# Optimization experiments

Hardware: AMD Instinct MI355X
Metric: run time of the kernel (lower is better)

## Reference

```python
import jax, jax.numpy as jnp
import numpy as np

EMBED = 1024
HEADS = 16
HEAD_DIM = 64
FF = 4096
EPS = 1e-5


def _layernorm(x, g, b):
    mu = jnp.mean(x, axis=-1, keepdims=True)
    var = jnp.mean(jnp.square(x - mu), axis=-1, keepdims=True)
    return (x - mu) * jax.lax.rsqrt(var + EPS) * g + b


def setup_inputs() -> dict:
    key = jax.random.key(0)
    ks = jax.random.split(key, 12)
    s_in = 1.0 / np.sqrt(EMBED)
    s_hd = 1.0 / np.sqrt(HEADS * HEAD_DIM)
    s_ff = 1.0 / np.sqrt(FF)
    return {
        "x": jax.random.normal(ks[0], (4, 2048, EMBED), dtype=jnp.float32),
        "Wq": jax.random.uniform(ks[1], (HEADS, EMBED, HEAD_DIM), jnp.float32, -s_in, s_in),
        "Wk": jax.random.uniform(ks[2], (HEADS, EMBED, HEAD_DIM), jnp.float32, -s_in, s_in),
        "Wv": jax.random.uniform(ks[3], (HEADS, EMBED, HEAD_DIM), jnp.float32, -s_in, s_in),
        "Wo": jax.random.uniform(ks[4], (HEADS * HEAD_DIM, EMBED), jnp.float32, -s_hd, s_hd),
        "bo": jax.random.uniform(ks[5], (EMBED,), jnp.float32, -s_hd, s_hd),
        "W1": jax.random.uniform(ks[6], (EMBED, FF), jnp.float32, -s_in, s_in),
        "b1": jax.random.uniform(ks[7], (FF,), jnp.float32, -s_in, s_in),
        "W2": jax.random.uniform(ks[8], (FF, EMBED), jnp.float32, -s_ff, s_ff),
        "b2": jax.random.uniform(ks[9], (EMBED,), jnp.float32, -s_ff, s_ff),
        "ln1_g": jnp.ones((EMBED,), jnp.float32),
        "ln1_b": jnp.zeros((EMBED,), jnp.float32),
        "ln2_g": jnp.ones((EMBED,), jnp.float32),
        "ln2_b": jnp.zeros((EMBED,), jnp.float32),
    }


def reference(x, Wq, Wk, Wv, Wo, bo, W1, b1, W2, b2, ln1_g, ln1_b, ln2_g, ln2_b):
    B, T, C = x.shape
    h = _layernorm(x, ln1_g, ln1_b)
    # per-head projections, batched over heads: [B,H,T,Dh]
    q = jnp.einsum("btc,hcd->bhtd", h, Wq)
    k = jnp.einsum("btc,hcd->bhtd", h, Wk)
    v = jnp.einsum("btc,hcd->bhtd", h, Wv)
    scale = HEAD_DIM ** -0.5
    att = jnp.einsum("bhtd,bhsd->bhts", q, k) * scale  # [B,H,T,T]
    causal = jnp.tril(jnp.ones((T, T), dtype=bool))
    att = jnp.where(causal, att, -jnp.inf)
    att = jax.nn.softmax(att, axis=-1)
    out = jnp.einsum("bhts,bhsd->bhtd", att, v)  # [B,H,T,Dh]
    # concat heads (matches torch.cat over head outputs) -> [B,T,H*Dh]
    out = out.transpose(0, 2, 1, 3).reshape(B, T, HEADS * HEAD_DIM)
    x = x + out @ Wo + bo
    h2 = _layernorm(x, ln2_g, ln2_b)
    ff = jax.nn.relu(h2 @ W1 + b1) @ W2 + b2
    return x + ff
```

## Files before the change

kernel.cpp:

```cpp
#include <hip/hip_runtime.h>
#include <hip/hip_bf16.h>

#define EMBED 1024
#define HEADS 16
#define HEAD_DIM 64
#define FFDIM 4096
#define TSEQ 2048
#define BATCH 4
#define ROWS (BATCH * TSEQ)

typedef __bf16 bf16;
typedef __attribute__((ext_vector_type(8))) __bf16 bf16x8;
typedef __attribute__((ext_vector_type(4))) __bf16 bf16x4;
typedef __attribute__((ext_vector_type(4))) float f32x4;

typedef const __attribute__((address_space(1))) void* gvp;
typedef __attribute__((address_space(3))) void* svp;

__global__ __launch_bounds__(256) void conv_wqkv_t(
    const float* __restrict__ Wq, const float* __restrict__ Wk,
    const float* __restrict__ Wv, bf16* __restrict__ WqkvT) {
  __shared__ bf16 t[64][72];
  int tid = threadIdx.x;
  int k0 = blockIdx.x * 64;
  int head = blockIdx.y;
  int which = blockIdx.z;
  const float* src = which == 0 ? Wq : which == 1 ? Wk : Wv;
  float scale = which == 0 ? 0.125f * 1.44269504088896f : 1.0f;
  src += (size_t)head * 65536;
  bf16* dst = WqkvT + ((size_t)which * 1024 + head * 64) * 1024;
#pragma unroll
  for (int i = 0; i < 4; ++i) {
    int r = i * 16 + (tid >> 4);
    int c = (tid & 15) * 4;
    float4 v = *(const float4*)&src[(size_t)(k0 + r) * 64 + c];
    t[c + 0][r] = (bf16)(v.x * scale);
    t[c + 1][r] = (bf16)(v.y * scale);
    t[c + 2][r] = (bf16)(v.z * scale);
    t[c + 3][r] = (bf16)(v.w * scale);
  }
  __syncthreads();
#pragma unroll
  for (int i = 0; i < 2; ++i) {
    int r = i * 32 + (tid >> 3);
    int c = (tid & 7) * 8;
    bf16x8 o;
#pragma unroll
    for (int j = 0; j < 8; ++j) o[j] = t[r][c + j];
    *(bf16x8*)&dst[(size_t)r * 1024 + k0 + c] = o;
  }
}

__global__ __launch_bounds__(256) void transpose_conv(
    const float* __restrict__ W, bf16* __restrict__ WT, int K, int N) {
  __shared__ bf16 t[64][72];
  int tid = threadIdx.x;
  int n0 = blockIdx.x * 64, k0 = blockIdx.y * 64;
#pragma unroll
  for (int i = 0; i < 4; ++i) {
    int r = i * 16 + (tid >> 4);
    int c = (tid & 15) * 4;
    float4 v = *(const float4*)&W[(size_t)(k0 + r) * N + n0 + c];
    t[c + 0][r] = (bf16)v.x;
    t[c + 1][r] = (bf16)v.y;
    t[c + 2][r] = (bf16)v.z;
    t[c + 3][r] = (bf16)v.w;
  }
  __syncthreads();
#pragma unroll
  for (int i = 0; i < 2; ++i) {
    int r = i * 32 + (tid >> 3);
    int c = (tid & 7) * 8;
    bf16x8 o;
#pragma unroll
    for (int j = 0; j < 8; ++j) o[j] = t[r][c + j];
    *(bf16x8*)&WT[(size_t)(n0 + r) * K + k0 + c] = o;
  }
}

__global__ __launch_bounds__(256) void transpose_v(const bf16* __restrict__ v,
                                                   bf16* __restrict__ vt) {
  __shared__ bf16 t[64][72];
  int bh = blockIdx.y;
  int t0 = blockIdx.x * 64;
  const bf16* src = v + (size_t)bh * 131072;
  bf16* dst = vt + (size_t)bh * 131072;
  int tid = threadIdx.x;
#pragma unroll
  for (int i = 0; i < 2; ++i) {
    int c = tid + i * 256;
    int r = c >> 3, d0 = (c & 7) * 8;
    bf16x8 vv = *(const bf16x8*)&src[(size_t)(t0 + r) * 64 + d0];
#pragma unroll
    for (int j = 0; j < 8; ++j) t[d0 + j][r] = vv[j];
  }
  __syncthreads();
#pragma unroll
  for (int i = 0; i < 2; ++i) {
    int c = tid + i * 256;
    int r = c >> 3, s0 = (c & 7) * 8;
    bf16x8 o;
#pragma unroll
    for (int j = 0; j < 8; ++j) o[j] = t[r][s0 + j];
    *(bf16x8*)&dst[(size_t)r * 2048 + t0 + s0] = o;
  }
}

__global__ __launch_bounds__(256) void ln_kernel(
    const float* __restrict__ x, const float* __restrict__ g,
    const float* __restrict__ bta, bf16* __restrict__ out) {
  int row = blockIdx.x;
  const float* xr = x + (size_t)row * EMBED;
  float4 v = ((const float4*)xr)[threadIdx.x];
  float s1 = v.x + v.y + v.z + v.w;
  float s2 = v.x * v.x + v.y * v.y + v.z * v.z + v.w * v.w;
#pragma unroll
  for (int off = 1; off < 64; off <<= 1) {
    s1 += __shfl_xor(s1, off);
    s2 += __shfl_xor(s2, off);
  }
  __shared__ float red[8];
  int wid = threadIdx.x >> 6;
  int lane = threadIdx.x & 63;
  if (lane == 0) {
    red[wid * 2] = s1;
    red[wid * 2 + 1] = s2;
  }
  __syncthreads();
  s1 = red[0] + red[2] + red[4] + red[6];
  s2 = red[1] + red[3] + red[5] + red[7];
  float mu = s1 * (1.0f / EMBED);
  float var = s2 * (1.0f / EMBED) - mu * mu;
  float rs = rsqrtf(var + 1e-5f);
  float4 gv = ((const float4*)g)[threadIdx.x];
  float4 bv = ((const float4*)bta)[threadIdx.x];
  bf16x4 o;
  o[0] = (bf16)((v.x - mu) * rs * gv.x + bv.x);
  o[1] = (bf16)((v.y - mu) * rs * gv.y + bv.y);
  o[2] = (bf16)((v.z - mu) * rs * gv.z + bv.z);
  o[3] = (bf16)((v.w - mu) * rs * gv.w + bv.w);
  *(bf16x4*)(out + (size_t)row * EMBED + threadIdx.x * 4) = o;
}

template <int EPI>
__global__ __launch_bounds__(256) void gemm_bf16(
    const bf16* __restrict__ A, const bf16* __restrict__ BT,
    float* __restrict__ Cf, bf16* __restrict__ Cb,
    const float* __restrict__ bias, const float* __restrict__ resid,
    int M, int N, int K) {
  __shared__ __attribute__((aligned(16))) bf16 As[128 * 32];
  __shared__ __attribute__((aligned(16))) bf16 Bs[128 * 32];
  int gx = gridDim.x;
  int nwg = gx * gridDim.y;
  int wgid = blockIdx.y * gx + blockIdx.x;
  int cpx = nwg >> 3;
  int swz = (wgid & 7) * cpx + (wgid >> 3);
  int m0 = (swz / gx) * 128, n0 = (swz % gx) * 128;
  int tid = threadIdx.x;
  int lane = tid & 63, wid = tid >> 6;
  int lr = lane & 15, lg = lane >> 4;
  int wr = (wid >> 1) * 64, wc = (wid & 1) * 64;
  int srow = lane >> 2;
  int sk = (lane & 3) * 8;
  f32x4 acc[4][4] = {};
  for (int kt = 0; kt < K; kt += 32) {
#pragma unroll
    for (int i = 0; i < 2; ++i) {
      int c = wid * 2 + i;
      int row = c * 16 + srow;
      const bf16* ga = &A[(size_t)(m0 + row) * K + kt + sk];
      const bf16* gb = &BT[(size_t)(n0 + row) * K + kt + sk];
      __builtin_amdgcn_global_load_lds((gvp)(const void*)ga,
                                       (svp)(void*)&As[c * 512], 16, 0, 0);
      __builtin_amdgcn_global_load_lds((gvp)(const void*)gb,
                                       (svp)(void*)&Bs[c * 512], 16, 0, 0);
    }
    __syncthreads();
    bf16x8 af[4], bfr[4];
#pragma unroll
    for (int i = 0; i < 4; ++i) {
      af[i] = *(const bf16x8*)&As[(wr + i * 16 + lr) * 32 + lg * 8];
      bfr[i] = *(const bf16x8*)&Bs[(wc + i * 16 + lr) * 32 + lg * 8];
    }
#pragma unroll
    for (int ar = 0; ar < 4; ++ar)
#pragma unroll
      for (int br = 0; br < 4; ++br)
        acc[ar][br] = __builtin_amdgcn_mfma_f32_16x16x32_bf16(
            af[ar], bfr[br], acc[ar][br], 0, 0, 0);
    __syncthreads();
  }
#pragma unroll
  for (int ar = 0; ar < 4; ++ar) {
#pragma unroll
    for (int br = 0; br < 4; ++br) {
#pragma unroll
      for (int r = 0; r < 4; ++r) {
        int row = m0 + wr + ar * 16 + lg * 4 + r;
        int col = n0 + wc + br * 16 + lr;
        float v = acc[ar][br][r];
        if (EPI == 0) {
          int which = col >> 10, cc = col & 1023;
          int b = row >> 11, t = row & 2047, h = cc >> 6, d = cc & 63;
          bf16* dst = Cb + (size_t)which * 8388608;
          dst[((size_t)((b << 4) + h) * TSEQ + t) * HEAD_DIM + d] = (bf16)v;
        } else if (EPI == 2) {
          size_t o = (size_t)row * N + col;
          Cf[o] = resid[o] + bias[col] + v;
        } else {
          size_t o = (size_t)row * N + col;
          float u = v + bias[col];
          Cb[o] = (bf16)(u > 0.f ? u : 0.f);
        }
      }
    }
  }
}

__global__ __launch_bounds__(256) void attn_kernel(
    const bf16* __restrict__ q, const bf16* __restrict__ k,
    const bf16* __restrict__ vt, bf16* __restrict__ out) {
  __shared__ __attribute__((aligned(16))) bf16 Ks[64][68];
  __shared__ __attribute__((aligned(16))) bf16 Vs[64][68];
  __shared__ __attribute__((aligned(16))) bf16 Ps[4][32][68];
  int bh = blockIdx.x;
  int b = bh >> 4, h = bh & 15;
  const bf16* qb = q + (size_t)bh * TSEQ * HEAD_DIM;
  const bf16* kb = k + (size_t)bh * TSEQ * HEAD_DIM;
  const bf16* vb = vt + (size_t)bh * HEAD_DIM * TSEQ;
  int tid = threadIdx.x, lane = tid & 63, w = tid >> 6;
  int lr = lane & 15, lg = lane >> 4;
  int Q = 15 - blockIdx.y;
  int tw = Q * 128 + w * 32;
  bf16x8 aq[2][2];
#pragma unroll
  for (int rg = 0; rg < 2; ++rg)
#pragma unroll
    for (int kc = 0; kc < 2; ++kc)
      aq[rg][kc] = *(const bf16x8*)&qb[(size_t)(tw + rg * 16 + lr) * HEAD_DIM +
                                       kc * 32 + lg * 8];
  f32x4 o[2][4] = {};
  float lrow[2][4] = {};
  int nj = 2 * Q + 2;
  for (int j = 0; j < nj; ++j) {
#pragma unroll
    for (int i = 0; i < 2; ++i) {
      int c = tid + i * 256;
      int rr = c >> 3, ko = (c & 7) * 8;
      *(bf16x8*)&Ks[rr][ko] =
          *(const bf16x8*)&kb[(size_t)(j * 64 + rr) * HEAD_DIM + ko];
      *(bf16x8*)&Vs[rr][ko] =
          *(const bf16x8*)&vb[(size_t)rr * TSEQ + j * 64 + ko];
    }
    __syncthreads();
    f32x4 s[2][4] = {};
#pragma unroll
    for (int nb = 0; nb < 4; ++nb) {
#pragma unroll
      for (int kc = 0; kc < 2; ++kc) {
        bf16x8 bk = *(const bf16x8*)&Ks[nb * 16 + lr][kc * 32 + lg * 8];
        s[0][nb] = __builtin_amdgcn_mfma_f32_16x16x32_bf16(aq[0][kc], bk,
                                                           s[0][nb], 0, 0, 0);
        s[1][nb] = __builtin_amdgcn_mfma_f32_16x16x32_bf16(aq[1][kc], bk,
                                                           s[1][nb], 0, 0, 0);
      }
    }
    if (j >= 2 * Q) {
#pragma unroll
      for (int rg = 0; rg < 2; ++rg)
#pragma unroll
        for (int nb = 0; nb < 4; ++nb)
#pragma unroll
          for (int r = 0; r < 4; ++r) {
            int sg = j * 64 + nb * 16 + lr;
            int tg = tw + rg * 16 + lg * 4 + r;
            if (sg > tg) s[rg][nb][r] = -1e30f;
          }
    }
#pragma unroll
    for (int rg = 0; rg < 2; ++rg) {
      float p[4][4];
#pragma unroll
      for (int r = 0; r < 4; ++r) {
        float su = 0.f;
#pragma unroll
        for (int nb = 0; nb < 4; ++nb) {
          p[nb][r] = exp2f(s[rg][nb][r] - 8.0f);
          su += p[nb][r];
        }
#pragma unroll
        for (int off = 1; off < 16; off <<= 1) su += __shfl_xor(su, off);
        lrow[rg][r] += su;
      }
#pragma unroll
      for (int nb = 0; nb < 4; ++nb)
#pragma unroll
        for (int r = 0; r < 4; ++r)
          Ps[w][rg * 16 + lg * 4 + r][nb * 16 + lr] = (bf16)p[nb][r];
    }
#pragma unroll
    for (int kc = 0; kc < 2; ++kc) {
      bf16x8 pa0 = *(const bf16x8*)&Ps[w][lr][kc * 32 + lg * 8];
      bf16x8 pa1 = *(const bf16x8*)&Ps[w][16 + lr][kc * 32 + lg * 8];
#pragma unroll
      for (int br = 0; br < 4; ++br) {
        bf16x8 bv = *(const bf16x8*)&Vs[br * 16 + lr][kc * 32 + lg * 8];
        o[0][br] =
            __builtin_amdgcn_mfma_f32_16x16x32_bf16(pa0, bv, o[0][br], 0, 0, 0);
        o[1][br] =
            __builtin_amdgcn_mfma_f32_16x16x32_bf16(pa1, bv, o[1][br], 0, 0, 0);
      }
    }
    __syncthreads();
  }
#pragma unroll
  for (int rg = 0; rg < 2; ++rg)
#pragma unroll
    for (int br = 0; br < 4; ++br)
#pragma unroll
      for (int r = 0; r < 4; ++r) {
        int t = tw + rg * 16 + lg * 4 + r;
        int d = br * 16 + lr;
        float val = o[rg][br][r] / lrow[rg][r];
        out[((size_t)(b * TSEQ) + t) * EMBED + h * HEAD_DIM + d] = (bf16)val;
      }
}

extern "C" void kernel_launch(void* const* d_in, const int* in_sizes, int n_in,
                              void* d_out, int out_size, void* d_ws,
                              size_t ws_size, hipStream_t stream) {
  const float* x = (const float*)d_in[0];
  const float* Wq = (const float*)d_in[1];
  const float* Wk = (const float*)d_in[2];
  const float* Wv = (const float*)d_in[3];
  const float* Wo = (const float*)d_in[4];
  const float* bo = (const float*)d_in[5];
  const float* W1 = (const float*)d_in[6];
  const float* b1 = (const float*)d_in[7];
  const float* W2 = (const float*)d_in[8];
  const float* b2 = (const float*)d_in[9];
  const float* g1 = (const float*)d_in[10];
  const float* be1 = (const float*)d_in[11];
  const float* g2 = (const float*)d_in[12];
  const float* be2 = (const float*)d_in[13];
  float* out = (float*)d_out;
  char* ws = (char*)d_ws;

  const size_t U = 16777216;
  bf16* h = (bf16*)(ws + 0 * U);
  bf16* qb = (bf16*)(ws + 1 * U);
  bf16* vtb = (bf16*)(ws + 0 * U);
  bf16* vnb = (bf16*)(ws + 3 * U);
  bf16* ao = (bf16*)(ws + 3 * U);
  float* x1 = (float*)(ws + 4 * U);
  bf16* h2 = (bf16*)(ws + 6 * U);
  bf16* ff1 = (bf16*)(ws + 0 * U);
  char* wbase = ws + 7 * U;
  bf16* WqkvT = (bf16*)(wbase);
  bf16* WoT = (bf16*)(wbase + 6291456);
  bf16* W1T = (bf16*)(wbase + 8388608);
  bf16* W2T = (bf16*)(wbase + 16777216);

  hipLaunchKernelGGL(conv_wqkv_t, dim3(16, 16, 3), dim3(256), 0, stream, Wq,
                     Wk, Wv, WqkvT);
  hipLaunchKernelGGL(transpose_conv, dim3(16, 16), dim3(256), 0, stream, Wo,
                     WoT, 1024, 1024);
  hipLaunchKernelGGL(transpose_conv, dim3(64, 16), dim3(256), 0, stream, W1,
                     W1T, 1024, 4096);
  hipLaunchKernelGGL(transpose_conv, dim3(16, 64), dim3(256), 0, stream, W2,
                     W2T, 4096, 1024);
  hipLaunchKernelGGL(ln_kernel, dim3(8192), dim3(256), 0, stream, x, g1, be1,
                     h);
  hipLaunchKernelGGL((gemm_bf16<0>), dim3(24, 64), dim3(256), 0, stream, h,
                     WqkvT, (float*)nullptr, qb, (const float*)nullptr,
                     (const float*)nullptr, ROWS, 3072, 1024);
  hipLaunchKernelGGL(transpose_v, dim3(32, 64), dim3(256), 0, stream, vnb,
                     vtb);
  hipLaunchKernelGGL(attn_kernel, dim3(64, 16), dim3(256), 0, stream, qb,
                     qb + 8388608, vtb, ao);
  hipLaunchKernelGGL((gemm_bf16<2>), dim3(8, 64), dim3(256), 0, stream, ao,
                     WoT, x1, (bf16*)nullptr, bo, x, ROWS, 1024, 1024);
  hipLaunchKernelGGL(ln_kernel, dim3(8192), dim3(256), 0, stream, x1, g2, be2,
                     h2);
  hipLaunchKernelGGL((gemm_bf16<3>), dim3(32, 64), dim3(256), 0, stream, h2,
                     W1T, (float*)nullptr, ff1, b1, (const float*)nullptr,
                     ROWS, 4096, 1024);
  hipLaunchKernelGGL((gemm_bf16<2>), dim3(8, 64), dim3(256), 0, stream, ff1,
                     W2T, out, (bf16*)nullptr, b2, x1, ROWS, 1024, 4096);
}
```

Baseline: 465.6 us.

## Add 256x256-tile triple-buffered GEMM with direct-to-LDS loads for QKV and FF1

Adds a new 512-thread GEMM kernel with 256x256 output tiles and a three-stage LDS ring filled by global_load_lds, using an XOR-swizzled layout and raised wave priority around the MFMA block. The QKV projection and the first FFN GEMM now use it, while the older 128x128 kernel is kept only for the residual-add epilogue. The larger tiles raise arithmetic intensity and the deeper pipeline overlaps loads with compute. In exchange the kernel uses 96KB of LDS and many accumulator registers, which limits occupancy. Grids are also small (384 and 512 blocks), so wave quantization across CUs is a risk.

```diff
diff --git a/kernel.cpp b/kernel.cpp
--- a/kernel.cpp
+++ b/kernel.cpp
@@ -143,11 +143,101 @@
 }
 
 template <int EPI>
+__global__ __launch_bounds__(512, 2) void gemm256(
+    const bf16* __restrict__ A, const bf16* __restrict__ BT,
+    bf16* __restrict__ Cb, const float* __restrict__ bias, int M, int N,
+    int K) {
+  __shared__ __attribute__((aligned(16))) char lds[98304];
+  int gx = gridDim.x;
+  int nwg = gx * gridDim.y;
+  int wgid = blockIdx.y * gx + blockIdx.x;
+  int cpx = nwg >> 3;
+  int swz = (wgid & 7) * cpx + (wgid >> 3);
+  int m0 = (swz / gx) * 256, n0 = (swz % gx) * 256;
+  int tid = threadIdx.x;
+  int lane = tid & 63, wid = tid >> 6;
+  int lr = lane & 15, lg = lane >> 4;
+  int wrM = (wid >> 2) * 128;
+  int wcN = (wid & 3) * 64;
+  int crow = lane >> 2;
+  int slotg = (lane & 3) ^ (crow & 3);
+  int NT = K >> 5;
+  size_t rb = (size_t)K * 2;
+
+  auto stageT = [&](int t) {
+    char* dst = lds + ((unsigned)t % 3u) * 32768u;
+#pragma unroll
+    for (int q = 0; q < 2; ++q) {
+      int c = wid * 2 + q;
+      const char* srcA = (const char*)A + (size_t)(m0 + c * 16 + crow) * rb +
+                         (size_t)t * 64 + slotg * 16;
+      __builtin_amdgcn_global_load_lds((gvp)srcA, (svp)(dst + c * 1024), 16, 0,
+                                       0);
+      const char* srcB = (const char*)BT + (size_t)(n0 + c * 16 + crow) * rb +
+                         (size_t)t * 64 + slotg * 16;
+      __builtin_amdgcn_global_load_lds((gvp)srcB, (svp)(dst + 16384 + c * 1024),
+                                       16, 0, 0);
+    }
+  };
+
+  stageT(0);
+  stageT(1);
+  f32x4 acc[8][4] = {};
+  int swcol = ((lg ^ (lr & 3)) * 16);
+  for (int t = 0; t < NT; ++t) {
+    asm volatile("s_waitcnt vmcnt(4)" ::: "memory");
+    __builtin_amdgcn_s_barrier();
+    const char* Ab = lds + ((unsigned)t % 3u) * 32768u;
+    const char* Bb = Ab + 16384;
+    bf16x8 af[8], bfr[4];
+#pragma unroll
+    for (int j = 0; j < 4; ++j)
+      bfr[j] = *(const bf16x8*)(Bb + (wcN + j * 16 + lr) * 64 + swcol);
+#pragma unroll
+    for (int i = 0; i < 8; ++i)
+      af[i] = *(const bf16x8*)(Ab + (wrM + i * 16 + lr) * 64 + swcol);
+    int tn = t + 2;
+    stageT(tn < NT ? tn : tn - NT);
+    __builtin_amdgcn_s_setprio(1);
+#pragma unroll
+    for (int i = 0; i < 8; ++i)
+#pragma unroll
+      for (int j = 0; j < 4; ++j)
+        acc[i][j] = __builtin_amdgcn_mfma_f32_16x16x32_bf16(af[i], bfr[j],
+                                                            acc[i][j], 0, 0, 0);
+    __builtin_amdgcn_s_setprio(0);
+  }
+  asm volatile("s_waitcnt vmcnt(0)" ::: "memory");
+#pragma unroll
+  for (int i = 0; i < 8; ++i) {
+#pragma unroll
+    for (int j = 0; j < 4; ++j) {
+#pragma unroll
+      for (int r = 0; r < 4; ++r) {
+        int row = m0 + wrM + i * 16 + lg * 4 + r;
+        int col = n0 + wcN + j * 16 + lr;
+        float v = acc[i][j][r];
+        if (EPI == 0) {
+          int which = col >> 10, cc = col & 1023;
+          int b = row >> 11, tt = row & 2047, h = cc >> 6, d = cc & 63;
+          bf16* dst = Cb + (size_t)which * 8388608;
+          dst[((size_t)((b << 4) + h) * TSEQ + tt) * HEAD_DIM + d] = (bf16)v;
+        } else {
+          size_t o = (size_t)row * N + col;
+          float u = v + bias[col];
+          Cb[o] = (bf16)(u > 0.f ? u : 0.f);
+        }
+      }
+    }
+  }
+}
+
+template <int EPI>
 __global__ __launch_bounds__(256) void gemm_bf16(
     const bf16* __restrict__ A, const bf16* __restrict__ BT,
     float* __restrict__ Cf, bf16* __restrict__ Cb,
-    const float* __restrict__ bias, const float* __restrict__ resid,
-    int M, int N, int K) {
+    const float* __restrict__ bias, const float* __restrict__ resid, int M,
+    int N, int K) {
   __shared__ __attribute__((aligned(16))) bf16 As[128 * 32];
   __shared__ __attribute__((aligned(16))) bf16 Bs[128 * 32];
   int gx = gridDim.x;
@@ -199,19 +289,8 @@
         int row = m0 + wr + ar * 16 + lg * 4 + r;
         int col = n0 + wc + br * 16 + lr;
         float v = acc[ar][br][r];
-        if (EPI == 0) {
-          int which = col >> 10, cc = col & 1023;
-          int b = row >> 11, t = row & 2047, h = cc >> 6, d = cc & 63;
-          bf16* dst = Cb + (size_t)which * 8388608;
-          dst[((size_t)((b << 4) + h) * TSEQ + t) * HEAD_DIM + d] = (bf16)v;
-        } else if (EPI == 2) {
-          size_t o = (size_t)row * N + col;
-          Cf[o] = resid[o] + bias[col] + v;
-        } else {
-          size_t o = (size_t)row * N + col;
-          float u = v + bias[col];
-          Cb[o] = (bf16)(u > 0.f ? u : 0.f);
-        }
+        size_t o = (size_t)row * N + col;
+        Cf[o] = resid[o] + bias[col] + v;
       }
     }
   }
@@ -371,9 +450,8 @@
                      W2T, 4096, 1024);
   hipLaunchKernelGGL(ln_kernel, dim3(8192), dim3(256), 0, stream, x, g1, be1,
                      h);
-  hipLaunchKernelGGL((gemm_bf16<0>), dim3(24, 64), dim3(256), 0, stream, h,
-                     WqkvT, (float*)nullptr, qb, (const float*)nullptr,
-                     (const float*)nullptr, ROWS, 3072, 1024);
+  hipLaunchKernelGGL((gemm256<0>), dim3(12, 32), dim3(512), 0, stream, h,
+                     WqkvT, qb, (const float*)nullptr, ROWS, 3072, 1024);
   hipLaunchKernelGGL(transpose_v, dim3(32, 64), dim3(256), 0, stream, vnb,
                      vtb);
   hipLaunchKernelGGL(attn_kernel, dim3(64, 16), dim3(256), 0, stream, qb,
@@ -382,9 +460,8 @@
                      WoT, x1, (bf16*)nullptr, bo, x, ROWS, 1024, 1024);
   hipLaunchKernelGGL(ln_kernel, dim3(8192), dim3(256), 0, stream, x1, g2, be2,
                      h2);
-  hipLaunchKernelGGL((gemm_bf16<3>), dim3(32, 64), dim3(256), 0, stream, h2,
-                     W1T, (float*)nullptr, ff1, b1, (const float*)nullptr,
-                     ROWS, 4096, 1024);
+  hipLaunchKernelGGL((gemm256<3>), dim3(16, 32), dim3(512), 0, stream, h2, W1T,
+                     ff1, b1, ROWS, 4096, 1024);
   hipLaunchKernelGGL((gemm_bf16<2>), dim3(8, 64), dim3(256), 0, stream, ff1,
                      W2T, out, (bf16*)nullptr, b2, x1, ROWS, 1024, 4096);
 }
```

After: 466.2 us. About the same (+0.1%).
